# Kernel tuning notes

Hardware: AMD Instinct MI355X
Metric: run time of the kernel (lower is better)

The kernel has to match this reference:

```python
import jax, jax.numpy as jnp
import numpy as np

# module config (matches init_kwargs)
H, W, C = 32, 32, 3
KH, KW, KC = 4, 4, 1
N_CLASS = 10
NBIN = 200
SHIFT = (0, 0)
NH, NW, NC = H // KH, W // KW, C // KC
NKERNEL = NH * NW * NC          # 192
NDIM_SUB = KH * KW * KC         # 16
NCOMP = NDIM_SUB                # n_component defaults to ndim_sub
NDIM = H * W * C                # 3072
NTRANS = NKERNEL * NCOMP        # 3072
N = 2048


def setup_inputs() -> dict:
    key = jax.random.key(0)
    k1, k2, k3, k4, k5, k6 = jax.random.split(key, 6)
    data = jax.random.normal(k1, (N, NDIM), dtype=jnp.float32)
    label = jax.random.randint(k2, (N,), 0, N_CLASS)
    # per-patch orthonormal projections: QR with sign fix, as in __init__
    wi = jax.random.normal(k3, (NKERNEL, NDIM_SUB, NCOMP), dtype=jnp.float32)
    Q, R = jnp.linalg.qr(wi)
    sign = jnp.sign(jnp.diagonal(R, axis1=-2, axis2=-1))
    wT_blocks = Q * sign[:, None, :]
    # monotone rational-quadratic spline knots per class / transformed dim
    dx = jax.random.uniform(k4, (N_CLASS, NTRANS, NBIN - 1), minval=0.5, maxval=1.5)
    dy = jax.random.uniform(k5, (N_CLASS, NTRANS, NBIN - 1), minval=0.5, maxval=1.5)
    z = jnp.zeros((N_CLASS, NTRANS, 1), jnp.float32)
    knots_x = -4.0 + 8.0 * jnp.concatenate([z, jnp.cumsum(dx, -1)], -1) / jnp.sum(dx, -1, keepdims=True)
    knots_y = -4.0 + 8.0 * jnp.concatenate([z, jnp.cumsum(dy, -1)], -1) / jnp.sum(dy, -1, keepdims=True)
    knots_d = jax.random.uniform(k6, (N_CLASS, NTRANS, NBIN), minval=0.5, maxval=1.5)
    return {"data": data, "label": label, "wT_blocks": wT_blocks,
            "knots_x": knots_x.astype(jnp.float32), "knots_y": knots_y.astype(jnp.float32),
            "knots_d": knots_d}


def construct_wT(wT_blocks):
    """Assemble block-structured (NDIM, NTRANS) projection from per-patch blocks."""
    dim = jnp.arange(NDIM).reshape(H, W, C)
    dim = jnp.roll(dim, (-SHIFT[0], -SHIFT[1]), axis=(0, 1))  # Shift() == negative roll
    # rows[b] = flat pixel indices of patch b; block order index = h*NW*NC + w*NC + c
    rows = dim.reshape(NH, KH, NW, KW, C).transpose(0, 2, 4, 1, 3).reshape(NKERNEL, NDIM_SUB)
    cols = jnp.arange(NKERNEL)[:, None] * NCOMP + jnp.arange(NCOMP)[None, :]
    wT = jnp.zeros((NDIM, NTRANS), wT_blocks.dtype)
    return wT.at[rows[:, :, None], cols[:, None, :]].set(wT_blocks)


def rq_spline(x, xx, yy, dd):
    """Monotone rational-quadratic spline with linear extrapolation.
    x: (N, T); xx/yy/dd: (T, K) knot positions / values / derivatives.
    Returns (y, log|dy/dx|), each (N, T)."""
    xT = x.T  # (T, N)
    lo, hi = xx[:, :1], xx[:, -1:]
    below, above = xT < lo, xT > hi
    xc = jnp.clip(xT, lo, hi)  # keep interior branch NaN-free
    k = jax.vmap(lambda kn, v: jnp.searchsorted(kn, v, side='right'))(xx, xc) - 1
    k = jnp.clip(k, 0, NBIN - 2)
    take = lambda a, i: jnp.take_along_axis(a, i, axis=1)
    xk, xk1 = take(xx, k), take(xx, k + 1)
    yk, yk1 = take(yy, k), take(yy, k + 1)
    dk, dk1 = take(dd, k), take(dd, k + 1)
    wdt = xk1 - xk
    s = (yk1 - yk) / wdt
    xi = (xc - xk) / wdt
    om = 1.0 - xi
    denom = s + (dk1 + dk - 2.0 * s) * xi * om
    ys = yk + (yk1 - yk) * (s * xi * xi + dk * xi * om) / denom
    lj_s = 2.0 * jnp.log(s) + jnp.log(dk1 * xi * xi + 2.0 * s * xi * om + dk * om * om) - 2.0 * jnp.log(denom)
    d0, dK = dd[:, :1], dd[:, -1:]
    y = jnp.where(below, yy[:, :1] + (xT - lo) * d0,
                  jnp.where(above, yy[:, -1:] + (xT - hi) * dK, ys))
    lj = jnp.where(below, jnp.log(d0), jnp.where(above, jnp.log(dK), lj_s))
    return y.T, lj.T


def reference(data, label, wT_blocks, knots_x, knots_y, knots_d):
    wT = construct_wT(wT_blocks)                 # (NDIM, NTRANS)
    data0 = data @ wT                            # (N, NTRANS)
    remaining = data - data0 @ wT.T              # orthogonal complement (zero here since full-rank)

    def body(carry, params):
        c, data1, logj = carry
        xx, yy, dd = params
        y, lj = rq_spline(data0, xx, yy, dd)
        m = label == c
        data1 = jnp.where(m[:, None], y, data1)
        logj = jnp.where(m, jnp.sum(lj, axis=1), logj)
        return (c + 1, data1, logj), None

    init = (jnp.int32(0), jnp.zeros_like(data0), jnp.zeros((data.shape[0],), data.dtype))
    (_, data1, logj), _ = jax.lax.scan(body, init, (knots_x, knots_y, knots_d))
    out = remaining + data1 @ wT.T
    return out, logj
```

## Files before the change

### kernel.cpp

```cpp
#include <hip/hip_runtime.h>

constexpr int NSAMP  = 2048;
constexpr int NDIM   = 3072;
constexpr int NTRANS = 3072;
constexpr int NBIN   = 200;
constexpr int NCLASS = 10;
constexpr int NPATCH = 192;
constexpr int BLK    = 256;
constexpr int PER_T  = NDIM / BLK;
constexpr int DSTR   = 20;
constexpr int SA     = 4;
constexpr int SC     = 4;

__device__ __forceinline__ float4* xb_line(float* xb, int p, int sl) {
    return (float4*)(xb + ((size_t)p * NSAMP + (sl ^ (p & 63))) * 16);
}
__device__ __forceinline__ const float4* xb_line_c(const float* xb, int p, int sl) {
    return (const float4*)(xb + ((size_t)p * NSAMP + (sl ^ (p & 63))) * 16);
}

__global__ __launch_bounds__(1024)
void p0_prep(const int* __restrict__ label,
             const float* __restrict__ B,
             int* __restrict__ slot,
             int* __restrict__ cls_off,
             float* __restrict__ Bt)
{
    __shared__ int s_lab[NSAMP];
    __shared__ int s_cnt[32][NCLASS];
    __shared__ int s_pre[32][NCLASS];
    __shared__ int s_tot[NCLASS];
    __shared__ int s_off[NCLASS + 1];
    const int tid  = threadIdx.x;
    const int lane = tid & 63;
    const int wv   = tid >> 6;

    for (int i = tid; i < NSAMP; i += 1024) s_lab[i] = label[i];
    for (int e = tid; e < NPATCH * 256; e += 1024) {
        const int p = e >> 8, r = e & 255;
        Bt[p * 256 + (r & 15) * 16 + (r >> 4)] = B[e];
    }
    __syncthreads();

    const unsigned long long ltmask = ((unsigned long long)1 << lane) - 1;
    int myrank[2], myc[2];
    #pragma unroll
    for (int pass = 0; pass < 2; ++pass) {
        const int n = pass * 1024 + tid;
        const int c = s_lab[n];
        myc[pass] = c;
        int r = 0;
        #pragma unroll
        for (int cls = 0; cls < NCLASS; ++cls) {
            const unsigned long long b = __ballot(c == cls);
            if (lane == 0) s_cnt[pass * 16 + wv][cls] = __popcll(b);
            if (cls == c)  r = __popcll(b & ltmask);
        }
        myrank[pass] = r;
    }
    __syncthreads();

    if (tid < 32 * NCLASS) {
        const int seg = tid & 31;
        const int cls = tid >> 5;
        int acc = 0;
        for (int s = 0; s < seg; ++s) acc += s_cnt[s][cls];
        s_pre[seg][cls] = acc;
        if (seg == 31) s_tot[cls] = acc + s_cnt[31][cls];
    }
    __syncthreads();
    if (tid == 0) {
        int a = 0;
        for (int c = 0; c < NCLASS; ++c) { s_off[c] = a; a += s_tot[c]; }
        s_off[NCLASS] = a;
    }
    __syncthreads();

    #pragma unroll
    for (int pass = 0; pass < 2; ++pass) {
        const int n   = pass * 1024 + tid;
        const int seg = pass * 16 + wv;
        const int c   = myc[pass];
        slot[n] = s_off[c] + s_pre[seg][c] + myrank[pass];
    }
    if (tid <= NCLASS) cls_off[tid] = s_off[tid];
}

__global__ __launch_bounds__(BLK, 4)
void pA_project(const float* __restrict__ data,
                const float* __restrict__ Bt,
                const int*   __restrict__ slot,
                float* __restrict__ xb)
{
    __shared__ float s_data[SA][NDIM];
    const int b   = blockIdx.x;
    const int tid = threadIdx.x;
    const int n0  = b * SA;

    #pragma unroll
    for (int s = 0; s < SA; ++s) {
        const float4* dr = (const float4*)(data + (size_t)(n0 + s) * NDIM);
        float4* sd = (float4*)s_data[s];
        #pragma unroll
        for (int j = 0; j < 3; ++j)
            sd[tid + BLK * j] = dr[tid + BLK * j];
    }
    int sls[SA];
    #pragma unroll
    for (int s = 0; s < SA; ++s) sls[s] = slot[n0 + s];
    __syncthreads();

    #pragma unroll 1
    for (int jj = 0; jj < 3; ++jj) {
        const int tau = tid + BLK * jj;
        const int p   = tau >> 2;
        const int q4  = tau & 3;
        const int nh  = p / 24;
        const int rem = p - nh * 24;
        const int nw  = rem / 3;
        const int ch  = rem - nw * 3;
        const int rowbase = nh * 384 + nw * 12 + ch;

        float4 Bp[16];
        const float4* Bg = (const float4*)(Bt + p * 256 + q4 * 64);
        #pragma unroll
        for (int i = 0; i < 16; ++i) Bp[i] = Bg[i];

        #pragma unroll
        for (int s = 0; s < SA; ++s) {
            float dv[16];
            #pragma unroll
            for (int i = 0; i < 16; ++i)
                dv[i] = s_data[s][rowbase + (i >> 2) * 96 + (i & 3) * 3];

            float acc[4];
            #pragma unroll
            for (int cc = 0; cc < 4; ++cc) {
                float a = 0.f;
                #pragma unroll
                for (int q = 0; q < 4; ++q) {
                    const float4 bv = Bp[cc * 4 + q];
                    a += bv.x * dv[q * 4 + 0] + bv.y * dv[q * 4 + 1]
                       + bv.z * dv[q * 4 + 2] + bv.w * dv[q * 4 + 3];
                }
                acc[cc] = a;
            }
            *(xb_line(xb, p, sls[s]) + q4) =
                make_float4(acc[0], acc[1], acc[2], acc[3]);
        }
    }
}

__global__ __launch_bounds__(BLK, 8)
void pB_spline(const float* __restrict__ kx,
               const float* __restrict__ ky,
               const float* __restrict__ kd,
               const int*   __restrict__ cls_off,
               float* __restrict__ xb,
               float* __restrict__ ljpart)
{
    __shared__ float s_kx[16 * NBIN];

    const int p   = blockIdx.x;
    const int c   = blockIdx.y;
    const int tid = threadIdx.x;
    const int t0  = p * 16;

    const size_t kofs = ((size_t)c * NTRANS + t0) * NBIN;
    const float4* gx = (const float4*)(kx + kofs);
    float4* lx = (float4*)s_kx;
    #pragma unroll 1
    for (int i = tid; i < 16 * NBIN / 4; i += BLK) lx[i] = gx[i];
    __syncthreads();

    const int qq  = tid & 3;
    const int sid = tid >> 2;
    const float* sxx = s_kx + qq * 4 * NBIN;
    const float* kyp = ky + kofs + (size_t)(qq * 4) * NBIN;
    const float* kdp = kd + kofs + (size_t)(qq * 4) * NBIN;

    const int beg = cls_off[c];
    const int end = cls_off[c + 1];

    for (int s0 = beg; s0 < end; s0 += 64) {
        const int sl = s0 + sid;
        if (sl < end) {
            float4* line = xb_line(xb, p, sl) + qq;
            const float4 v = *line;
            float xs[4] = {v.x, v.y, v.z, v.w};

            float lj_sum = 0.f;
            #pragma unroll
            for (int j = 0; j < 4; ++j) {
                const float* xx  = sxx + j * NBIN;
                const float* yyg = kyp + j * NBIN;
                const float* ddg = kdp + j * NBIN;
                const float x  = xs[j];
                const float lo = xx[0];
                const float hi = xx[NBIN - 1];

                float y, lj;
                if (x < lo) {
                    const float d0 = ddg[0];
                    y  = yyg[0] + (x - lo) * d0;
                    lj = __logf(d0);
                } else if (x > hi) {
                    const float dK = ddg[NBIN - 1];
                    y  = yyg[NBIN - 1] + (x - hi) * dK;
                    lj = __logf(dK);
                } else {
                    int klo = 0, khi = NBIN;
                    #pragma unroll
                    for (int it = 0; it < 8; ++it) {
                        const int mid = (klo + khi) >> 1;
                        const bool le = (xx[mid] <= x);
                        klo = le ? mid : klo;
                        khi = le ? khi : mid;
                    }
                    int k = klo;
                    if (k > NBIN - 2) k = NBIN - 2;

                    const float xk = xx[k], xk1 = xx[k + 1];
                    const float yk = yyg[k], yk1 = yyg[k + 1];
                    const float dk = ddg[k], dk1 = ddg[k + 1];

                    const float wdt     = xk1 - xk;
                    const float inv_wdt = __fdividef(1.f, wdt);
                    const float dy      = yk1 - yk;
                    const float s       = dy * inv_wdt;
                    const float xi      = (x - xk) * inv_wdt;
                    const float om      = 1.f - xi;
                    const float denom   = s + (dk1 + dk - 2.f * s) * xi * om;
                    const float r       = __fdividef(1.f, denom);
                    const float num     = dy * (s * xi * xi + dk * xi * om);
                    y = yk + num * r;
                    const float Nq = dk1 * xi * xi + 2.f * s * xi * om + dk * om * om;
                    const float t2 = s * r;
                    lj = __logf(t2 * t2 * Nq);
                }
                xs[j] = y - x;
                lj_sum += lj;
            }

            *line = make_float4(xs[0], xs[1], xs[2], xs[3]);

            lj_sum += __shfl_xor(lj_sum, 1);
            lj_sum += __shfl_xor(lj_sum, 2);
            if (qq == 0) ljpart[(size_t)p * NSAMP + sl] = lj_sum;
        }
    }
}

__global__ __launch_bounds__(BLK)
void p_ljred(const float* __restrict__ ljpart,
             float* __restrict__ logj_slot)
{
    const int sl = blockIdx.x * BLK + threadIdx.x;
    float a0 = 0.f, a1 = 0.f, a2 = 0.f, a3 = 0.f;
    #pragma unroll 1
    for (int g = 0; g < NPATCH; g += 4) {
        a0 += ljpart[(size_t)(g + 0) * NSAMP + sl];
        a1 += ljpart[(size_t)(g + 1) * NSAMP + sl];
        a2 += ljpart[(size_t)(g + 2) * NSAMP + sl];
        a3 += ljpart[(size_t)(g + 3) * NSAMP + sl];
    }
    logj_slot[sl] = (a0 + a1) + (a2 + a3);
}

__global__ __launch_bounds__(BLK, 2)
void pC_recon(const float* __restrict__ data,
              const float* __restrict__ B,
              const int*   __restrict__ slot,
              const float* __restrict__ xb,
              const float* __restrict__ logj_slot,
              float* __restrict__ out,
              float* __restrict__ logj)
{
    __shared__ float s_diff[SC][NPATCH * DSTR];
    const int b   = blockIdx.x;
    const int tid = threadIdx.x;
    const int n0  = b * SC;

    #pragma unroll
    for (int s = 0; s < SC; ++s) {
        const int sl = slot[n0 + s];
        #pragma unroll
        for (int jj = 0; jj < 3; ++jj) {
            const int i  = tid + BLK * jj;
            const int pp = i >> 2;
            const int q  = i & 3;
            const float4 v = *(xb_line_c(xb, pp, sl) + q);
            *(float4*)&s_diff[s][pp * DSTR + q * 4] = v;
        }
    }
    if (tid < SC) logj[n0 + tid] = logj_slot[slot[n0 + tid]];
    __syncthreads();

    #pragma unroll 1
    for (int j = 0; j < PER_T; ++j) {
        const int d  = tid + BLK * j;
        const int ch = d % 3;
        const int hw = d / 3;
        const int w  = hw & 31;
        const int h  = hw >> 5;
        const int p  = ((h >> 2) * 8 + (w >> 2)) * 3 + ch;
        const int i  = (h & 3) * 4 + (w & 3);

        const float4* Bp4 = (const float4*)(B + p * 256 + i * 16);
        const float4 b0 = Bp4[0], b1 = Bp4[1], b2 = Bp4[2], b3 = Bp4[3];

        #pragma unroll
        for (int s = 0; s < SC; ++s) {
            const float4* dp4 = (const float4*)&s_diff[s][p * DSTR];
            const float4 d0 = dp4[0], d1 = dp4[1], d2 = dp4[2], d3 = dp4[3];
            float acc = data[(size_t)(n0 + s) * NDIM + d];
            acc += b0.x * d0.x + b0.y * d0.y + b0.z * d0.z + b0.w * d0.w;
            acc += b1.x * d1.x + b1.y * d1.y + b1.z * d1.z + b1.w * d1.w;
            acc += b2.x * d2.x + b2.y * d2.y + b2.z * d2.z + b2.w * d2.w;
            acc += b3.x * d3.x + b3.y * d3.y + b3.z * d3.z + b3.w * d3.w;
            out[(size_t)(n0 + s) * NDIM + d] = acc;
        }
    }
}

extern "C" void kernel_launch(void* const* d_in, const int* in_sizes, int n_in,
                              void* d_out, int out_size, void* d_ws, size_t ws_size,
                              hipStream_t stream) {
    const float* data  = (const float*)d_in[0];
    const int*   label = (const int*)  d_in[1];
    const float* B     = (const float*)d_in[2];
    const float* kx    = (const float*)d_in[3];
    const float* ky    = (const float*)d_in[4];
    const float* kd    = (const float*)d_in[5];

    float* out  = (float*)d_out;
    float* logj = (float*)d_out + (size_t)NSAMP * NDIM;

    char* ws = (char*)d_ws;
    size_t off = 0;
    float* xb        = (float*)(ws + off); off += (size_t)NPATCH * NSAMP * 16 * 4;
    float* ljpart    = (float*)(ws + off); off += (size_t)NPATCH * NSAMP * 4;
    float* Bt        = (float*)(ws + off); off += (size_t)NPATCH * 256 * 4;
    float* logj_slot = (float*)(ws + off); off += NSAMP * 4;
    int*   slot      = (int*)  (ws + off); off += NSAMP * 4;
    int*   cls_off   = (int*)  (ws + off); off += 64;

    p0_prep   <<<1, 1024, 0, stream>>>(label, B, slot, cls_off, Bt);
    pA_project<<<NSAMP / SA, BLK, 0, stream>>>(data, Bt, slot, xb);
    dim3 gridB(NPATCH, NCLASS);
    pB_spline <<<gridB, BLK, 0, stream>>>(kx, ky, kd, cls_off, xb, ljpart);
    p_ljred   <<<NSAMP / BLK, BLK, 0, stream>>>(ljpart, logj_slot);
    pC_recon  <<<NSAMP / SC, BLK, 0, stream>>>(data, B, slot, xb, logj_slot, out, logj);
}
```

Measured before the change: 236.8 us.

## Add per-dimension knot lookup table to shorten spline bin search

Each spline block now builds a 128-cell byte lookup table in shared memory that maps a uniform grid over [-4,4] to knot indices. The per-sample binary search starts from the narrow range this table gives, so it takes 3 dependent shared-memory probes instead of 8. The cost is an extra table-building phase with a serial scan and one more barrier per block. It also assumes knots spread across [-4,4] with few knots per cell; denser knots would make the 3-step search wrong.

```diff
diff --git a/kernel.cpp b/kernel.cpp
--- a/kernel.cpp
+++ b/kernel.cpp
@@ -11,6 +11,8 @@
 constexpr int DSTR   = 20;
 constexpr int SA     = 4;
 constexpr int SC     = 4;
+constexpr int NL     = 128;
+constexpr int LUTS   = 136;
 
 __device__ __forceinline__ float4* xb_line(float* xb, int p, int sl) {
     return (float4*)(xb + ((size_t)p * NSAMP + (sl ^ (p & 63))) * 16);
@@ -160,6 +162,7 @@
                float* __restrict__ ljpart)
 {
     __shared__ float s_kx[16 * NBIN];
+    __shared__ unsigned char s_lut[16 * LUTS];
 
     const int p   = blockIdx.x;
     const int c   = blockIdx.y;
@@ -171,6 +174,32 @@
     float4* lx = (float4*)s_kx;
     #pragma unroll 1
     for (int i = tid; i < 16 * NBIN / 4; i += BLK) lx[i] = gx[i];
+    __syncthreads();
+
+    {
+        const int r  = tid >> 4;
+        const int ch = tid & 15;
+        const float* xx = s_kx + r * NBIN;
+        const int j0 = ch * 8;
+        const float xu0 = -4.0f + (float)j0 * (8.0f / NL);
+        int klo = 0, khi = NBIN;
+        #pragma unroll
+        for (int it = 0; it < 8; ++it) {
+            const int mid = (klo + khi) >> 1;
+            const bool le = (xx[mid] <= xu0);
+            klo = le ? mid : klo;
+            khi = le ? khi : mid;
+        }
+        int k = klo;
+        const int nj = (ch == 15) ? 9 : 8;
+        unsigned char* lrow = s_lut + r * LUTS + j0;
+        #pragma unroll 1
+        for (int jj = 0; jj < nj; ++jj) {
+            const float xuj = -4.0f + (float)(j0 + jj) * (8.0f / NL);
+            while (k < NBIN - 1 && xx[k + 1] <= xuj) ++k;
+            lrow[jj] = (unsigned char)k;
+        }
+    }
     __syncthreads();
 
     const int qq  = tid & 3;
@@ -195,6 +224,7 @@
                 const float* xx  = sxx + j * NBIN;
                 const float* yyg = kyp + j * NBIN;
                 const float* ddg = kdp + j * NBIN;
+                const unsigned char* lrow = s_lut + (qq * 4 + j) * LUTS;
                 const float x  = xs[j];
                 const float lo = xx[0];
                 const float hi = xx[NBIN - 1];
@@ -209,9 +239,14 @@
                     y  = yyg[NBIN - 1] + (x - hi) * dK;
                     lj = __logf(dK);
                 } else {
-                    int klo = 0, khi = NBIN;
+                    int u = (int)((x + 4.0f) * (NL / 8.0f));
+                    u = u < 0 ? 0 : (u > NL - 1 ? NL - 1 : u);
+                    int klo = (int)lrow[u] - 1;
+                    klo = klo < 0 ? 0 : klo;
+                    int khi = (int)lrow[u + 1] + 2;
+                    khi = khi > NBIN ? NBIN : khi;
                     #pragma unroll
-                    for (int it = 0; it < 8; ++it) {
+                    for (int it = 0; it < 3; ++it) {
                         const int mid = (klo + khi) >> 1;
                         const bool le = (xx[mid] <= x);
                         klo = le ? mid : klo;
```

After: 239.8 us. No clear change (+1.3%).
